# Kernel tuning notes

Measured on AMD Instinct MI355X. Metric: run time of the kernel, lower is better.

Reference implementation:

```python
import jax, jax.numpy as jnp
import numpy as np

B, S, D, H, DK, FF = 2, 2048, 1024, 16, 64, 4096
EPS = 1e-6


def _layernorm(x, g, b):
    m = jnp.mean(x, axis=-1, keepdims=True)
    v = jnp.mean((x - m) ** 2, axis=-1, keepdims=True)
    return (x - m) * jax.lax.rsqrt(v + EPS) * g + b


def setup_inputs() -> dict:
    key = jax.random.key(0)
    ks = jax.random.split(key, 20)
    sc = 0.02
    rn = lambda k, sh: (jax.random.normal(k, sh, jnp.float32) * sc)
    return {
        "inputs": jax.random.normal(ks[0], (B, S, D), jnp.float32),
        "wq": rn(ks[1], (D, H * DK)), "bq": jnp.zeros((H * DK,), jnp.float32),
        "wk": rn(ks[2], (D, H * DK)), "bk": jnp.zeros((H * DK,), jnp.float32),
        "wv": rn(ks[3], (D, H * DK)), "bv": jnp.zeros((H * DK,), jnp.float32),
        "wo": rn(ks[4], (H * DK, D)), "bo": jnp.zeros((D,), jnp.float32),
        "ln1_g": jnp.ones((D,), jnp.float32), "ln1_b": jnp.zeros((D,), jnp.float32),
        "wi0": rn(ks[5], (D, FF)), "bi0": jnp.zeros((FF,), jnp.float32),
        "wi1": rn(ks[6], (D, FF)), "bi1": jnp.zeros((FF,), jnp.float32),
        "wff": rn(ks[7], (FF, D)), "bff": jnp.zeros((D,), jnp.float32),
        "ln2_g": jnp.ones((D,), jnp.float32), "ln2_b": jnp.zeros((D,), jnp.float32),
    }


def reference(inputs, wq, bq, wk, bk, wv, bv, wo, bo, ln1_g, ln1_b,
              wi0, bi0, wi1, bi1, wff, bff, ln2_g, ln2_b):
    # --- pre-norm MHA block ---
    h = _layernorm(inputs, ln1_g, ln1_b)
    q = (h @ wq + bq).reshape(B, S, H, DK)
    k = (h @ wk + bk).reshape(B, S, H, DK)
    v = (h @ wv + bv).reshape(B, S, H, DK)
    scores = jnp.einsum('bqhd,bkhd->bhqk', q, k) / jnp.sqrt(jnp.float32(DK))
    attn = jax.nn.softmax(scores, axis=-1)                 # [B,H,S,S]
    ctx = jnp.einsum('bhqk,bkhd->bqhd', attn, v).reshape(B, S, H * DK)
    h1 = inputs + (ctx @ wo + bo)
    # --- pre-norm GeGLU FFN block ---
    h2 = _layernorm(h1, ln2_g, ln2_b)
    hg = jax.nn.gelu(h2 @ wi0 + bi0, approximate=False)
    hl = h2 @ wi1 + bi1
    out = h1 + ((hg * hl) @ wff + bff)
    return out, attn
```

## Files before the change

### kernel.cpp

```cpp
#include <hip/hip_runtime.h>
#include <hip/hip_bf16.h>
#include <cstdint>

#define DEV __device__ __forceinline__

typedef __bf16 bf16_t;
typedef __bf16 bf16x8 __attribute__((ext_vector_type(8)));
typedef __bf16 bf16x4 __attribute__((ext_vector_type(4)));
typedef float  f32x4  __attribute__((ext_vector_type(4)));

constexpr int Bb = 2, Ss = 2048, Dd = 1024, Hh = 16, DKk = 64, FFf = 4096;
constexpr int TOK = Bb * Ss;
constexpr float LN_EPS = 1e-6f;

DEV void g2l16(const void* g, void* l) {
    __builtin_amdgcn_global_load_lds(
        (const __attribute__((address_space(1))) unsigned int*)g,
        (__attribute__((address_space(3))) unsigned int*)l, 16, 0, 0);
}

#define WAITCNT(N) asm volatile("s_waitcnt vmcnt(" #N ")" ::: "memory")
#define SCHEDB() __builtin_amdgcn_sched_barrier(0)

__global__ __launch_bounds__(256)
void transpose_all(const float* __restrict__ wq, const float* __restrict__ wk,
                   const float* __restrict__ wv, const float* __restrict__ wo,
                   const float* __restrict__ wi0, const float* __restrict__ wi1,
                   const float* __restrict__ wff,
                   bf16_t* wqT, bf16_t* wkT, bf16_t* wvT, bf16_t* woT,
                   bf16_t* wi0T, bf16_t* wi1T, bf16_t* wffT,
                   const float* __restrict__ bq, const float* __restrict__ bk,
                   const float* __restrict__ bv, float* __restrict__ cb) {
    __shared__ float t[32][33];
    const int id = blockIdx.x;
    if (id == 16384) {
        const int tid = threadIdx.x;
#pragma unroll
        for (int i = 0; i < 4; ++i) {
            const int j = i * 256 + tid;
            cb[j] = bq[j]; cb[1024 + j] = bk[j]; cb[2048 + j] = bv[j];
        }
        return;
    }
    const float* src; bf16_t* dst; int K, N, tt;
    if (id < 4096) {
        const int w = id >> 10; tt = id & 1023; K = 1024; N = 1024;
        src = w == 0 ? wq : w == 1 ? wk : w == 2 ? wv : wo;
        dst = w == 0 ? wqT : w == 1 ? wkT : w == 2 ? wvT : woT;
    } else if (id < 12288) {
        const int w = (id - 4096) >> 12; tt = (id - 4096) & 4095; K = 1024; N = 4096;
        src = w ? wi1 : wi0; dst = w ? wi1T : wi0T;
    } else {
        tt = id - 12288; K = 4096; N = 1024;
        src = wff; dst = wffT;
    }
    const int ntn = N >> 5;
    const int n0 = (tt % ntn) * 32, k0 = (tt / ntn) * 32;
    const int tx = threadIdx.x & 31, ty = threadIdx.x >> 5;
#pragma unroll
    for (int i = 0; i < 4; ++i)
        t[ty + 8 * i][tx] = src[(size_t)(k0 + ty + 8 * i) * N + n0 + tx];
    __syncthreads();
#pragma unroll
    for (int i = 0; i < 4; ++i)
        dst[(size_t)(n0 + ty + 8 * i) * K + k0 + tx] = (bf16_t)t[tx][ty + 8 * i];
}

__global__ __launch_bounds__(256)
void ln_fwd(const float* __restrict__ x, const float* __restrict__ g,
            const float* __restrict__ b, bf16_t* __restrict__ out) {
    __shared__ float red[8];
    const int row = blockIdx.x, tid = threadIdx.x;
    const float4 v = ((const float4*)(x + (size_t)row * Dd))[tid];
    float s  = v.x + v.y + v.z + v.w;
    float sq = v.x * v.x + v.y * v.y + v.z * v.z + v.w * v.w;
#pragma unroll
    for (int o = 32; o; o >>= 1) { s += __shfl_xor(s, o); sq += __shfl_xor(sq, o); }
    if ((tid & 63) == 0) { red[tid >> 6] = s; red[4 + (tid >> 6)] = sq; }
    __syncthreads();
    s  = red[0] + red[1] + red[2] + red[3];
    sq = red[4] + red[5] + red[6] + red[7];
    const float mean = s * (1.f / Dd);
    const float var  = sq * (1.f / Dd) - mean * mean;
    const float rs   = rsqrtf(var + LN_EPS);
    const float4 gv = ((const float4*)g)[tid];
    const float4 bv = ((const float4*)b)[tid];
    bf16x4 o4;
    o4[0] = (bf16_t)((v.x - mean) * rs * gv.x + bv.x);
    o4[1] = (bf16_t)((v.y - mean) * rs * gv.y + bv.y);
    o4[2] = (bf16_t)((v.z - mean) * rs * gv.z + bv.z);
    o4[3] = (bf16_t)((v.w - mean) * rs * gv.w + bv.w);
    ((bf16x4*)(out + (size_t)row * Dd))[tid] = o4;
}

template <int EPI>
DEV void gemm_epi(float val, int gr, int gc, int N, size_t zofs,
                  void* outp, void* out2, void* out3, const float* resid) {
    if constexpr (EPI == 0) {
        ((bf16_t*)outp)[(size_t)gr * N + gc] = (bf16_t)val;
    } else if constexpr (EPI == 1) {
        const size_t idx = (size_t)gr * N + gc;
        ((float*)outp)[idx] = val + resid[idx];
    } else if constexpr (EPI == 4) {
        ((float*)outp)[zofs + (size_t)gr * N + gc] = val;
    } else {
        const int sel = gc >> 10, col = gc & 1023;
        if (sel == 0) {
            ((bf16_t*)outp)[(size_t)gr * 1024 + col] = (bf16_t)val;
        } else if (sel == 1) {
            ((bf16_t*)out2)[(size_t)gr * 1024 + col] = (bf16_t)val;
        } else {
            const int bb = gr >> 11, sS = gr & 2047;
            ((bf16_t*)out3)[((size_t)bb << 21) + ((size_t)col << 11) + sS] = (bf16_t)val;
        }
    }
}

template <int BM, int BN, int EPI>
__global__ __launch_bounds__(256)
void gemm_t(const bf16_t* __restrict__ A, const bf16_t* __restrict__ Bt,
            const float* __restrict__ bias, const float* __restrict__ resid,
            void* __restrict__ outp, void* __restrict__ out2,
            void* __restrict__ out3, int M, int N, int K, int ld) {
    constexpr int WM = BM / 2, WN = BN / 2;
    constexpr int MI = WM / 16, NI = WN / 16;
    constexpr int CA = BM / 32, CB = BN / 32;
    __shared__ bf16_t As[BM * 64];
    __shared__ bf16_t Bs[BN * 64];
    const int tid = threadIdx.x;
    const int lane = tid & 63;
    const int wave = tid >> 6;
    const int wr = wave >> 1, wc = wave & 1;
    const int m0 = blockIdx.y * BM, n0 = blockIdx.x * BN;
    const int koff = blockIdx.z * K;
    const size_t zofs = (size_t)blockIdx.z * M * N;
    const int lr = lane & 15, lg = lane >> 4;

    const f32x4 z0 = {0.f, 0.f, 0.f, 0.f};
    f32x4 acc[MI][NI];
#pragma unroll
    for (int i = 0; i < MI; ++i)
#pragma unroll
        for (int j = 0; j < NI; ++j) acc[i][j] = z0;

    for (int k0 = 0; k0 < K; k0 += 64) {
#pragma unroll
        for (int c = 0; c < CA; ++c) {
            const int lin = c * 256 + tid;
            const int row = lin >> 3, col = (lin & 7) * 8;
            g2l16(A + (size_t)(m0 + row) * ld + koff + k0 + col, (char*)As + lin * 16);
        }
#pragma unroll
        for (int c = 0; c < CB; ++c) {
            const int lin = c * 256 + tid;
            const int row = lin >> 3, col = (lin & 7) * 8;
            g2l16(Bt + (size_t)(n0 + row) * ld + koff + k0 + col, (char*)Bs + lin * 16);
        }
        __syncthreads();

        bf16x8 af[2][MI], bw[2][NI];
#pragma unroll
        for (int kk = 0; kk < 2; ++kk)
#pragma unroll
            for (int mi = 0; mi < MI; ++mi)
                af[kk][mi] = *(const bf16x8*)(As + (wr * WM + mi * 16 + lr) * 64 +
                                              kk * 32 + lg * 8);
#pragma unroll
        for (int kk = 0; kk < 2; ++kk)
#pragma unroll
            for (int ni = 0; ni < NI; ++ni)
                bw[kk][ni] = *(const bf16x8*)(Bs + (wc * WN + ni * 16 + lr) * 64 +
                                              kk * 32 + lg * 8);
#pragma unroll
        for (int mi = 0; mi < MI; ++mi)
#pragma unroll
            for (int ni = 0; ni < NI; ++ni) {
                acc[mi][ni] = __builtin_amdgcn_mfma_f32_16x16x32_bf16(
                    af[0][mi], bw[0][ni], acc[mi][ni], 0, 0, 0);
                acc[mi][ni] = __builtin_amdgcn_mfma_f32_16x16x32_bf16(
                    af[1][mi], bw[1][ni], acc[mi][ni], 0, 0, 0);
            }
        __syncthreads();
    }

#pragma unroll
    for (int mi = 0; mi < MI; ++mi)
#pragma unroll
        for (int ni = 0; ni < NI; ++ni) {
            const int gc = n0 + wc * WN + ni * 16 + lr;
            const int gr0 = m0 + wr * WM + mi * 16 + lg * 4;
            const float bvl = (EPI == 4) ? 0.f : bias[gc];
#pragma unroll
            for (int r = 0; r < 4; ++r)
                gemm_epi<EPI>(acc[mi][ni][r] + bvl, gr0 + r, gc, N, zofs,
                              outp, out2, out3, resid);
        }
}

__global__ __launch_bounds__(256)
void reduce2(const float* __restrict__ part, const float* __restrict__ h1,
             const float* __restrict__ bff, float* __restrict__ out) {
    const int row = blockIdx.x, tid = threadIdx.x;
    const size_t idx = (size_t)row * 1024 + tid * 4;
    const float4 a = *(const float4*)(part + idx);
    const float4 b = *(const float4*)(part + (size_t)4096 * 1024 + idx);
    const float4 r = *(const float4*)(h1 + idx);
    const float4 bv = *(const float4*)(bff + tid * 4);
    float4 o;
    o.x = a.x + b.x + r.x + bv.x;
    o.y = a.y + b.y + r.y + bv.y;
    o.z = a.z + b.z + r.z + bv.z;
    o.w = a.w + b.w + r.w + bv.w;
    *(float4*)(out + idx) = o;
}

__global__ __launch_bounds__(256)
void gemm_geglu(const bf16_t* __restrict__ A, const bf16_t* __restrict__ Bg,
                const bf16_t* __restrict__ Bl, const float* __restrict__ bi0,
                const float* __restrict__ bi1, bf16_t* __restrict__ gout) {
    __shared__ bf16_t As[128 * 64];
    __shared__ bf16_t Bgs[64 * 64];
    __shared__ bf16_t Bls[64 * 64];
    const int tid = threadIdx.x;
    const int lane = tid & 63;
    const int wave = tid >> 6;
    const int wr = wave >> 1, wc = wave & 1;
    const int m0 = blockIdx.y * 128, n0 = blockIdx.x * 64;
    const int lr = lane & 15, lg = lane >> 4;

    const f32x4 z0 = {0.f, 0.f, 0.f, 0.f};
    f32x4 ag[4][2], al[4][2];
#pragma unroll
    for (int i = 0; i < 4; ++i)
#pragma unroll
        for (int j = 0; j < 2; ++j) { ag[i][j] = z0; al[i][j] = z0; }

    for (int k0 = 0; k0 < 1024; k0 += 64) {
#pragma unroll
        for (int c = 0; c < 4; ++c) {
            const int lin = c * 256 + tid;
            const int row = lin >> 3, col = (lin & 7) * 8;
            g2l16(A + (size_t)(m0 + row) * 1024 + k0 + col, (char*)As + lin * 16);
        }
#pragma unroll
        for (int c = 0; c < 2; ++c) {
            const int lin = c * 256 + tid;
            const int row = lin >> 3, col = (lin & 7) * 8;
            g2l16(Bg + (size_t)(n0 + row) * 1024 + k0 + col, (char*)Bgs + lin * 16);
        }
#pragma unroll
        for (int c = 0; c < 2; ++c) {
            const int lin = c * 256 + tid;
            const int row = lin >> 3, col = (lin & 7) * 8;
            g2l16(Bl + (size_t)(n0 + row) * 1024 + k0 + col, (char*)Bls + lin * 16);
        }
        __syncthreads();

        bf16x8 af[2][4], bg[2][2], bl[2][2];
#pragma unroll
        for (int kk = 0; kk < 2; ++kk) {
#pragma unroll
            for (int mi = 0; mi < 4; ++mi)
                af[kk][mi] = *(const bf16x8*)(As + (wr * 64 + mi * 16 + lr) * 64 +
                                              kk * 32 + lg * 8);
#pragma unroll
            for (int ni = 0; ni < 2; ++ni) {
                bg[kk][ni] = *(const bf16x8*)(Bgs + (wc * 32 + ni * 16 + lr) * 64 +
                                              kk * 32 + lg * 8);
                bl[kk][ni] = *(const bf16x8*)(Bls + (wc * 32 + ni * 16 + lr) * 64 +
                                              kk * 32 + lg * 8);
            }
        }
#pragma unroll
        for (int mi = 0; mi < 4; ++mi)
#pragma unroll
            for (int ni = 0; ni < 2; ++ni) {
#pragma unroll
                for (int kk = 0; kk < 2; ++kk) {
                    ag[mi][ni] = __builtin_amdgcn_mfma_f32_16x16x32_bf16(
                        af[kk][mi], bg[kk][ni], ag[mi][ni], 0, 0, 0);
                    al[mi][ni] = __builtin_amdgcn_mfma_f32_16x16x32_bf16(
                        af[kk][mi], bl[kk][ni], al[mi][ni], 0, 0, 0);
                }
            }
        __syncthreads();
    }

#pragma unroll
    for (int mi = 0; mi < 4; ++mi)
#pragma unroll
        for (int ni = 0; ni < 2; ++ni) {
            const int gc = n0 + wc * 32 + ni * 16 + lr;
            const int gr0 = m0 + wr * 64 + mi * 16 + lg * 4;
            const float b0 = bi0[gc], b1 = bi1[gc];
#pragma unroll
            for (int r = 0; r < 4; ++r) {
                const float x = ag[mi][ni][r] + b0;
                const float y = al[mi][ni][r] + b1;
                const float ge = 0.5f * x * (1.f + erff(x * 0.70710678118654752f));
                gout[(size_t)(gr0 + r) * 4096 + gc] = (bf16_t)(ge * y);
            }
        }
}

__global__ __launch_bounds__(512)
void attn_fused(const bf16_t* __restrict__ q, const bf16_t* __restrict__ k,
                const bf16_t* __restrict__ vT, float* __restrict__ attn,
                bf16_t* __restrict__ ctx) {
    __shared__ bf16_t lds[6 * 4096];
    const int tid = threadIdx.x, lane = tid & 63, wave = tid >> 6;
    const int lr = lane & 15, lg = lane >> 4;
    int blk = blockIdx.x;
    blk = (blk & 7) * 64 + (blk >> 3);
    const int qc = blk & 15, bh = blk >> 4;
    const int b = bh >> 4, h = bh & 15;
    const int q0 = qc * 128 + wave * 16;
    const size_t base = (size_t)b * (Ss * 1024) + h * 64;
    constexpr float SCL = 0.125f * 1.4426950408889634f;
    const f32x4 z0 = {0.f, 0.f, 0.f, 0.f};

    const int st_r8 = lane >> 3;
    const int st_c0 = (lane & 7) ^ (st_r8 & 3) ^ ((wave & 1) << 2);
    const int st_c0A = (lane & 7) ^ (st_r8 & 3);

    const bf16x8 aq0 = *(const bf16x8*)(q + base + (size_t)(q0 + lr) * 1024 + lg * 8);
    const bf16x8 aq1 = *(const bf16x8*)(q + base + (size_t)(q0 + lr) * 1024 + 32 + lg * 8);
    const bf16_t* kb = k + base;
    const bf16_t* vb_base = vT + ((size_t)bh * 64) * Ss;

#define STAGE_KA(kt_, buf_)                                                       \
    {                                                                             \
        g2l16(kb + (size_t)((kt_) * 128 + wave * 16 + st_r8) * 1024 + st_c0A * 8, \
              lds + (buf_) * 8192 + wave * 1024);                                 \
        g2l16(kb + (size_t)((kt_) * 128 + wave * 16 + 8 + st_r8) * 1024 +         \
                  (st_c0A ^ 4) * 8,                                               \
              lds + (buf_) * 8192 + wave * 1024 + 512);                           \
    }
#define STAGE_K(kt_, buf_)                                                        \
    g2l16(kb + (size_t)((kt_) * 64 + wave * 8 + st_r8) * 1024 + st_c0 * 8,        \
          lds + (buf_) * 4096 + wave * 512);
#define STAGE_V(kt_, buf_)                                                        \
    g2l16(vb_base + (size_t)(wave * 8 + st_r8) * Ss + (kt_) * 64 + st_c0 * 8,     \
          lds + (3 + (buf_)) * 4096 + wave * 512);

    f32x4 ea = z0, eb = z0;
    STAGE_KA(0, 0);
    STAGE_KA(1, 1);
    for (int kt = 0; kt < 16; ++kt) {
        const int buf = kt % 3;
        if (kt == 15) { WAITCNT(0); } else { WAITCNT(2); }
        SCHEDB();
        __builtin_amdgcn_s_barrier();
        SCHEDB();
        f32x4 sa[8];
        __builtin_amdgcn_s_setprio(1);
#pragma unroll
        for (int ct = 0; ct < 8; ++ct) {
            const int ar = ct * 16 + lr;
            const int hz = (ar & 3) | (((ar >> 3) & 1) << 2);
            bf16x8 k0 = *(const bf16x8*)&lds[buf * 8192 + ar * 64 + (lg ^ hz) * 8];
            bf16x8 k1 = *(const bf16x8*)&lds[buf * 8192 + ar * 64 + (((4 + lg) ^ hz)) * 8];
            sa[ct] = __builtin_amdgcn_mfma_f32_16x16x32_bf16(k0, aq0, z0, 0, 0, 0);
            sa[ct] = __builtin_amdgcn_mfma_f32_16x16x32_bf16(k1, aq1, sa[ct], 0, 0, 0);
        }
        __builtin_amdgcn_s_setprio(0);
#pragma unroll
        for (int r = 0; r < 4; ++r) {
            ea[r] += exp2f(sa[0][r] * SCL) + exp2f(sa[1][r] * SCL) +
                     exp2f(sa[2][r] * SCL) + exp2f(sa[3][r] * SCL);
            eb[r] += exp2f(sa[4][r] * SCL) + exp2f(sa[5][r] * SCL) +
                     exp2f(sa[6][r] * SCL) + exp2f(sa[7][r] * SCL);
        }
        if (kt + 2 < 16) STAGE_KA(kt + 2, (kt + 2) % 3);
    }
    float e = ((ea[0] + ea[1]) + (ea[2] + ea[3])) + ((eb[0] + eb[1]) + (eb[2] + eb[3]));
    e += __shfl_xor(e, 16);
    e += __shfl_xor(e, 32);
    const float invl = 1.f / e;

    f32x4 cacc[4];
#pragma unroll
    for (int nd = 0; nd < 4; ++nd) cacc[nd] = z0;

    float* attn_base = attn + ((size_t)bh * Ss + q0 + lr) * Ss;

    __builtin_amdgcn_s_barrier();
    SCHEDB();

    STAGE_K(0, 0); STAGE_V(0, 0);
    STAGE_K(1, 1); STAGE_V(1, 1);
    for (int kt = 0; kt < 32; ++kt) {
        const int buf = kt % 3;
        if (kt == 0) { WAITCNT(2); }
        else if (kt == 31) { WAITCNT(4); }
        else { WAITCNT(6); }
        SCHEDB();
        __builtin_amdgcn_s_barrier();
        SCHEDB();
#pragma unroll
        for (int kp = 0; kp < 2; ++kp) {
            bf16x8 pa;
            __builtin_amdgcn_s_setprio(1);
#pragma unroll
            for (int ch = 0; ch < 2; ++ch) {
                const int pr = kp * 32 + (lr >> 2) * 8 + ch * 4 + (lr & 3);
                const int hz = (pr & 3) | (((pr >> 3) & 1) << 2);
                bf16x8 k0 = *(const bf16x8*)&lds[buf * 4096 + pr * 64 + (lg ^ hz) * 8];
                bf16x8 k1 = *(const bf16x8*)&lds[buf * 4096 + pr * 64 + (((4 + lg) ^ hz)) * 8];
                f32x4 sb = __builtin_amdgcn_mfma_f32_16x16x32_bf16(k0, aq0, z0, 0, 0, 0);
                sb = __builtin_amdgcn_mfma_f32_16x16x32_bf16(k1, aq1, sb, 0, 0, 0);
                float4 p;
                p.x = exp2f(sb[0] * SCL) * invl;
                p.y = exp2f(sb[1] * SCL) * invl;
                p.z = exp2f(sb[2] * SCL) * invl;
                p.w = exp2f(sb[3] * SCL) * invl;
                *(float4*)(attn_base + kt * 64 + kp * 32 + lg * 8 + ch * 4) = p;
                pa[ch * 4 + 0] = (bf16_t)p.x;
                pa[ch * 4 + 1] = (bf16_t)p.y;
                pa[ch * 4 + 2] = (bf16_t)p.z;
                pa[ch * 4 + 3] = (bf16_t)p.w;
            }
#pragma unroll
            for (int nd = 0; nd < 4; ++nd) {
                const int vr = nd * 16 + lr;
                const int hv = (vr & 3) | (((vr >> 3) & 1) << 2);
                bf16x8 vb = *(const bf16x8*)&lds[(3 + buf) * 4096 + vr * 64 +
                                                 (((kp * 4 + lg) ^ hv)) * 8];
                cacc[nd] = __builtin_amdgcn_mfma_f32_16x16x32_bf16(pa, vb, cacc[nd], 0, 0, 0);
            }
            __builtin_amdgcn_s_setprio(0);
        }
        if (kt + 2 < 32) {
            const int nb = (kt + 2) % 3;
            STAGE_K(kt + 2, nb);
            STAGE_V(kt + 2, nb);
        }
    }
#pragma unroll
    for (int nd = 0; nd < 4; ++nd)
#pragma unroll
        for (int r = 0; r < 4; ++r)
            ctx[((size_t)b * Ss + q0 + lg * 4 + r) * 1024 + h * 64 + nd * 16 + lr] =
                (bf16_t)cacc[nd][r];
#undef STAGE_KA
#undef STAGE_K
#undef STAGE_V
}

extern "C" void kernel_launch(void* const* d_in, const int* in_sizes, int n_in,
                              void* d_out, int out_size, void* d_ws, size_t ws_size,
                              hipStream_t stream) {
    const float* inp  = (const float*)d_in[0];
    const float* wq   = (const float*)d_in[1];
    const float* bq   = (const float*)d_in[2];
    const float* wk   = (const float*)d_in[3];
    const float* bk   = (const float*)d_in[4];
    const float* wv   = (const float*)d_in[5];
    const float* bv   = (const float*)d_in[6];
    const float* wo   = (const float*)d_in[7];
    const float* bo   = (const float*)d_in[8];
    const float* ln1g = (const float*)d_in[9];
    const float* ln1b = (const float*)d_in[10];
    const float* wi0  = (const float*)d_in[11];
    const float* bi0  = (const float*)d_in[12];
    const float* wi1  = (const float*)d_in[13];
    const float* bi1  = (const float*)d_in[14];
    const float* wff  = (const float*)d_in[15];
    const float* bff  = (const float*)d_in[16];
    const float* ln2g = (const float*)d_in[17];
    const float* ln2b = (const float*)d_in[18];

    const size_t M1 = 1u << 20;
    bf16_t* wsb  = (bf16_t*)d_ws;
    bf16_t* wqT  = wsb + 0 * M1;
    bf16_t* wkT  = wsb + 1 * M1;
    bf16_t* wvT  = wsb + 2 * M1;
    bf16_t* woT  = wsb + 3 * M1;
    bf16_t* wi0T = wsb + 4 * M1;
    bf16_t* wi1T = wsb + 8 * M1;
    bf16_t* wffT = wsb + 12 * M1;
    bf16_t* hbuf = wsb + 16 * M1;
    bf16_t* qbuf = wsb + 20 * M1;
    bf16_t* kbuf = wsb + 24 * M1;
    bf16_t* vTb  = wsb + 28 * M1;
    bf16_t* ctxb = wsb + 32 * M1;
    float*  h1   = (float*)(wsb + 36 * M1);
    bf16_t* gbuf = wsb + 44 * M1;
    float*  part = (float*)(wsb + 20 * M1);
    float*  cb   = (float*)(wsb + 60 * M1);

    float* out  = (float*)d_out;
    float* attn = out + (size_t)TOK * Dd;

    transpose_all<<<16385, 256, 0, stream>>>(wq, wk, wv, wo, wi0, wi1, wff,
                                             wqT, wkT, wvT, woT, wi0T, wi1T, wffT,
                                             bq, bk, bv, cb);

    ln_fwd<<<TOK, 256, 0, stream>>>(inp, ln1g, ln1b, hbuf);

    gemm_t<128, 128, 3><<<dim3(24, 32), 256, 0, stream>>>(
        hbuf, wqT, cb, nullptr, qbuf, kbuf, vTb, TOK, 3072, 1024, 1024);

    attn_fused<<<Bb * Hh * (Ss / 128), 512, 0, stream>>>(qbuf, kbuf, vTb, attn, ctxb);

    gemm_t<64, 64, 1><<<dim3(16, 64), 256, 0, stream>>>(
        ctxb, woT, bo, inp, h1, nullptr, nullptr, TOK, 1024, 1024, 1024);

    ln_fwd<<<TOK, 256, 0, stream>>>(h1, ln2g, ln2b, hbuf);

    gemm_geglu<<<dim3(64, 32), 256, 0, stream>>>(hbuf, wi0T, wi1T, bi0, bi1, gbuf);

    gemm_t<128, 64, 4><<<dim3(16, 32, 2), 256, 0, stream>>>(
        gbuf, wffT, bff, nullptr, part, nullptr, nullptr, TOK, 1024, 2048, 4096);

    reduce2<<<4096, 256, 0, stream>>>(part, h1, bff, out);
}
```

Before: 470.2 us.

## Fuse first layernorm into weight prepass and stage V-transpose stores through LDS

Merges the first layernorm launch into the weight transpose/convert kernel as extra blocks, removing one kernel launch and its serialization. In the QKV GEMM, the transposed V output is now staged through shared memory so each thread writes contiguous 16-byte vectors along the sequence axis, instead of scattered 2-byte stores with a 4 KB stride. This adds an extra LDS round trip and a barrier in the V-producing blocks, and the shared tile buffer is reused for staging.

```diff
diff --git a/kernel.cpp b/kernel.cpp
--- a/kernel.cpp
+++ b/kernel.cpp
@@ -23,18 +23,45 @@
 #define SCHEDB() __builtin_amdgcn_sched_barrier(0)
 
 __global__ __launch_bounds__(256)
-void transpose_all(const float* __restrict__ wq, const float* __restrict__ wk,
-                   const float* __restrict__ wv, const float* __restrict__ wo,
-                   const float* __restrict__ wi0, const float* __restrict__ wi1,
-                   const float* __restrict__ wff,
-                   bf16_t* wqT, bf16_t* wkT, bf16_t* wvT, bf16_t* woT,
-                   bf16_t* wi0T, bf16_t* wi1T, bf16_t* wffT,
-                   const float* __restrict__ bq, const float* __restrict__ bk,
-                   const float* __restrict__ bv, float* __restrict__ cb) {
+void prepass(const float* __restrict__ wq, const float* __restrict__ wk,
+             const float* __restrict__ wv, const float* __restrict__ wo,
+             const float* __restrict__ wi0, const float* __restrict__ wi1,
+             const float* __restrict__ wff,
+             bf16_t* wqT, bf16_t* wkT, bf16_t* wvT, bf16_t* woT,
+             bf16_t* wi0T, bf16_t* wi1T, bf16_t* wffT,
+             const float* __restrict__ bq, const float* __restrict__ bk,
+             const float* __restrict__ bv, float* __restrict__ cb,
+             const float* __restrict__ x, const float* __restrict__ lg,
+             const float* __restrict__ lb, bf16_t* __restrict__ lnout) {
     __shared__ float t[32][33];
     const int id = blockIdx.x;
+    const int tid = threadIdx.x;
+    if (id >= 16385) {
+        __shared__ float red[8];
+        const int row = id - 16385;
+        const float4 v = ((const float4*)(x + (size_t)row * Dd))[tid];
+        float s  = v.x + v.y + v.z + v.w;
+        float sq = v.x * v.x + v.y * v.y + v.z * v.z + v.w * v.w;
+#pragma unroll
+        for (int o = 32; o; o >>= 1) { s += __shfl_xor(s, o); sq += __shfl_xor(sq, o); }
+        if ((tid & 63) == 0) { red[tid >> 6] = s; red[4 + (tid >> 6)] = sq; }
+        __syncthreads();
+        s  = red[0] + red[1] + red[2] + red[3];
+        sq = red[4] + red[5] + red[6] + red[7];
+        const float mean = s * (1.f / Dd);
+        const float var  = sq * (1.f / Dd) - mean * mean;
+        const float rs   = rsqrtf(var + LN_EPS);
+        const float4 gv = ((const float4*)lg)[tid];
+        const float4 bv2 = ((const float4*)lb)[tid];
+        bf16x4 o4;
+        o4[0] = (bf16_t)((v.x - mean) * rs * gv.x + bv2.x);
+        o4[1] = (bf16_t)((v.y - mean) * rs * gv.y + bv2.y);
+        o4[2] = (bf16_t)((v.z - mean) * rs * gv.z + bv2.z);
+        o4[3] = (bf16_t)((v.w - mean) * rs * gv.w + bv2.w);
+        ((bf16x4*)(lnout + (size_t)row * Dd))[tid] = o4;
+        return;
+    }
     if (id == 16384) {
-        const int tid = threadIdx.x;
 #pragma unroll
         for (int i = 0; i < 4; ++i) {
             const int j = i * 256 + tid;
@@ -56,7 +83,7 @@
     }
     const int ntn = N >> 5;
     const int n0 = (tt % ntn) * 32, k0 = (tt / ntn) * 32;
-    const int tx = threadIdx.x & 31, ty = threadIdx.x >> 5;
+    const int tx = tid & 31, ty = tid >> 5;
 #pragma unroll
     for (int i = 0; i < 4; ++i)
         t[ty + 8 * i][tx] = src[(size_t)(k0 + ty + 8 * i) * N + n0 + tx];
@@ -95,7 +122,7 @@
 
 template <int EPI>
 DEV void gemm_epi(float val, int gr, int gc, int N, size_t zofs,
-                  void* outp, void* out2, void* out3, const float* resid) {
+                  void* outp, void* out2, const float* resid) {
     if constexpr (EPI == 0) {
         ((bf16_t*)outp)[(size_t)gr * N + gc] = (bf16_t)val;
     } else if constexpr (EPI == 1) {
@@ -105,14 +132,8 @@
         ((float*)outp)[zofs + (size_t)gr * N + gc] = val;
     } else {
         const int sel = gc >> 10, col = gc & 1023;
-        if (sel == 0) {
-            ((bf16_t*)outp)[(size_t)gr * 1024 + col] = (bf16_t)val;
-        } else if (sel == 1) {
-            ((bf16_t*)out2)[(size_t)gr * 1024 + col] = (bf16_t)val;
-        } else {
-            const int bb = gr >> 11, sS = gr & 2047;
-            ((bf16_t*)out3)[((size_t)bb << 21) + ((size_t)col << 11) + sS] = (bf16_t)val;
-        }
+        if (sel == 0) ((bf16_t*)outp)[(size_t)gr * 1024 + col] = (bf16_t)val;
+        else          ((bf16_t*)out2)[(size_t)gr * 1024 + col] = (bf16_t)val;
     }
 }
 
@@ -125,8 +146,9 @@
     constexpr int WM = BM / 2, WN = BN / 2;
     constexpr int MI = WM / 16, NI = WN / 16;
     constexpr int CA = BM / 32, CB = BN / 32;
-    __shared__ bf16_t As[BM * 64];
-    __shared__ bf16_t Bs[BN * 64];
+    __shared__ bf16_t sh[BM * 64 + BN * 64];
+    bf16_t* As = sh;
+    bf16_t* Bs = sh + BM * 64;
     const int tid = threadIdx.x;
     const int lane = tid & 63;
     const int wave = tid >> 6;
@@ -183,6 +205,35 @@
         __syncthreads();
     }
 
+    if constexpr (EPI == 3) {
+        if (n0 >= 2048 && BM == 128 && BN == 128) {
+            bf16_t* tb = sh;
+#pragma unroll
+            for (int mi = 0; mi < MI; ++mi)
+#pragma unroll
+                for (int ni = 0; ni < NI; ++ni) {
+                    const int cl = wc * WN + ni * 16 + lr;
+                    const int rl0 = wr * WM + mi * 16 + lg * 4;
+                    const float bvl = bias[n0 + cl];
+#pragma unroll
+                    for (int r = 0; r < 4; ++r)
+                        tb[cl * 128 + rl0 + r] = (bf16_t)(acc[mi][ni][r] + bvl);
+                }
+            __syncthreads();
+            const int bb = m0 >> 11, s0 = m0 & 2047;
+            bf16_t* vout = (bf16_t*)out3 + ((size_t)bb << 21) + ((size_t)(n0 - 2048) << 11) + s0;
+            const int cl = tid >> 4;
+            const int sc = (tid & 15) * 8;
+#pragma unroll
+            for (int rnd = 0; rnd < 8; ++rnd) {
+                const int c = rnd * 16 + cl;
+                *(bf16x8*)(vout + ((size_t)c << 11) + sc) =
+                    *(const bf16x8*)(tb + c * 128 + sc);
+            }
+            return;
+        }
+    }
+
 #pragma unroll
     for (int mi = 0; mi < MI; ++mi)
 #pragma unroll
@@ -193,7 +244,7 @@
 #pragma unroll
             for (int r = 0; r < 4; ++r)
                 gemm_epi<EPI>(acc[mi][ni][r] + bvl, gr0 + r, gc, N, zofs,
-                              outp, out2, out3, resid);
+                              outp, out2, resid);
         }
 }
 
@@ -492,11 +543,10 @@
     float* out  = (float*)d_out;
     float* attn = out + (size_t)TOK * Dd;
 
-    transpose_all<<<16385, 256, 0, stream>>>(wq, wk, wv, wo, wi0, wi1, wff,
+    prepass<<<16385 + TOK, 256, 0, stream>>>(wq, wk, wv, wo, wi0, wi1, wff,
                                              wqT, wkT, wvT, woT, wi0T, wi1T, wffT,
-                                             bq, bk, bv, cb);
-
-    ln_fwd<<<TOK, 256, 0, stream>>>(inp, ln1g, ln1b, hbuf);
+                                             bq, bk, bv, cb,
+                                             inp, ln1g, ln1b, hbuf);
 
     gemm_t<128, 128, 3><<<dim3(24, 32), 256, 0, stream>>>(
         hbuf, wqT, cb, nullptr, qbuf, kbuf, vTb, TOK, 3072, 1024, 1024);
```

Result: faster. 456.1 us (-3.0%).
